# Kernel optimization log

Measured on AMD Instinct MI355X. Metric: run time of the kernel, lower is better.

The kernel has to match this reference:

```python
import jax, jax.numpy as jnp
import numpy as np

K = 5          # kernel_width of the predicted per-pixel kernels
PAD = K // 2   # Unfold padding
CONV_K = 3     # BaseNet: single 3x3 'same' conv, C -> C*K*K


def setup_inputs() -> dict:
    key = jax.random.key(0)
    k1, k2, k3 = jax.random.split(key, 3)
    N, C, H, W = 4, 16, 256, 256
    x = jax.random.normal(k1, (N, C, H, W), dtype=jnp.float32)
    fan_in = C * CONV_K * CONV_K
    conv_w = jax.random.normal(k2, (C * K * K, C, CONV_K, CONV_K), dtype=jnp.float32) / np.sqrt(fan_in).astype(np.float32)
    conv_b = jax.random.normal(k3, (C * K * K,), dtype=jnp.float32) * 0.01
    return {"x": x, "conv_w": conv_w, "conv_b": conv_b}


def _unfold(x):
    # torch.nn.Unfold(K, padding=K//2), reshaped to (N, C, K*K, H, W):
    # patches[n, c, i*K + j, h, w] = x_padded[n, c, h + i, w + j]
    # (channel-major, kernel positions row-major -- matches torch ordering)
    N, C, H, W = x.shape
    xp = jnp.pad(x, ((0, 0), (0, 0), (PAD, PAD), (PAD, PAD)))
    patches = jnp.stack(
        [xp[:, :, i:i + H, j:j + W] for i in range(K) for j in range(K)],
        axis=2,
    )
    return patches  # (N, C, K*K, H, W)


def reference(x, conv_w, conv_b):
    N, C, H, W = x.shape
    # BaseNet: 3x3 'same' conv predicting C*K*K logits per pixel
    out = jax.lax.conv_general_dilated(
        x, conv_w, window_strides=(1, 1), padding='SAME',
        dimension_numbers=('NCHW', 'OIHW', 'NCHW'),
    ) + conv_b[None, :, None, None]
    logits = out.reshape(N, C, K * K, H, W)
    weights = jax.nn.softmax(logits, axis=2)          # softmax over the K*K window
    # einsum('ncuij,ncuij->ncij'): per-pixel weighted sum over the window
    return jnp.einsum('ncuij,ncuij->ncij', _unfold(x), weights)
```

## Files before the change

kernel.cpp:

```cpp
#include <hip/hip_runtime.h>


typedef __bf16 bf16x8 __attribute__((ext_vector_type(8)));
typedef float  f32x16 __attribute__((ext_vector_type(16)));
typedef float  f32x4  __attribute__((ext_vector_type(4)));

#define IMG  256
#define C_IN 16

__device__ __forceinline__ unsigned short f2bf(float f) {
  union { float f; unsigned int u; } v; v.f = f;
  unsigned int u = v.u;
  return (unsigned short)((u + 0x7FFFu + ((u >> 16) & 1u)) >> 16);
}

__global__ __launch_bounds__(256, 2) void kpn_fused(
    const float* __restrict__ x, const float* __restrict__ cw,
    const float* __restrict__ cb, float* __restrict__ out)
{
  __shared__ unsigned short xclf[20 * 20 * 16];
  __shared__ unsigned short xep[20][20][18];
  __shared__ float2 pbl[32][8];

  const int tid  = threadIdx.x;
  const int w0   = blockIdx.x * 16;
  const int h0   = blockIdx.y * 16;
  const int nimg = blockIdx.z;

  {
    int cp = tid & 7, row = tid >> 3;
    float2 v;
    if (row < 25) { v.x = cb[(2 * cp) * 25 + row]; v.y = cb[(2 * cp + 1) * 25 + row]; }
    else          { v.x = -1e30f; v.y = -1e30f; }
    pbl[row][cp] = v;
  }

  char* xclb = (char*)xclf;
  for (int i = tid; i < 3200; i += 256) {
    int ci = i / 200, rem = i % 200, rr = rem / 10, c2 = rem % 10;
    int gh = h0 + rr - 2, gw = w0 + c2 * 2 - 2;
    float vx = 0.f, vy = 0.f;
    if (gh >= 0 && gh < IMG) {
      const float* rowp = x + ((nimg * C_IN + ci) * IMG + gh) * IMG;
      if (gw >= 0 && gw + 1 < IMG) { float2 v = *(const float2*)(rowp + gw); vx = v.x; vy = v.y; }
      else {
        if (gw >= 0 && gw < IMG)         vx = rowp[gw];
        if (gw + 1 >= 0 && gw + 1 < IMG) vy = rowp[gw + 1];
      }
    }
    unsigned short bx = f2bf(vx), by = f2bf(vy);
    int cc = c2 * 2, half = ci >> 3, cil = ci & 7;
    int q0 = rr * 20 + cc, q1 = q0 + 1;
    *(unsigned short*)(xclb + q0 * 32 + ((half ^ (q0 & 1)) << 4) + cil * 2) = bx;
    *(unsigned short*)(xclb + q1 * 32 + ((half ^ (q1 & 1)) << 4) + cil * 2) = by;
    xep[rr][cc][ci] = bx;
    xep[rr][cc + 1][ci] = by;
  }
  __syncthreads();

  const int wave  = tid >> 6;
  const int lane  = tid & 63;
  const int g     = lane >> 5;
  const int n32   = lane & 31;
  const int px    = n32 & 15;
  const int py_in = n32 >> 4;
  const int m     = n32;
  const bool mval = (m < 25);

  int offs[16];
#pragma unroll
  for (int r = 0; r < 16; ++r) {
    int row = 4 * g + (r & 3) + 8 * (r >> 2);
    int du = row / 5, dv = row % 5;
    offs[r] = (row < 25) ? ((du * 20 + dv) * 36) : 0;
  }

  const char* xepb = (const char*)&xep[0][0][0];

  auto epi = [&](const f32x16& A0, const f32x16& A1, int c0, int py) {
    const int cp = c0 >> 1;
    float s0 = 0.f, s1 = 0.f, ws0 = 0.f, ws1 = 0.f;
    const int base = (py * 20 + px) * 36 + c0 * 2;
#pragma unroll
    for (int r = 0; r < 16; ++r) {
      float2 b = pbl[4 * g + (r & 3) + 8 * (r >> 2)][cp];
      float e0 = __expf(A0[r] + b.x);
      float e1 = __expf(A1[r] + b.y);
      s0 += e0; s1 += e1;
      unsigned int u = *(const unsigned int*)(xepb + base + offs[r]);
      union { unsigned int u; float f; } lo, hi;
      lo.u = u << 16; hi.u = u & 0xFFFF0000u;
      ws0 = fmaf(e0, lo.f, ws0);
      ws1 = fmaf(e1, hi.f, ws1);
    }
    s0 += __shfl_xor(s0, 32); s1 += __shfl_xor(s1, 32);
    ws0 += __shfl_xor(ws0, 32); ws1 += __shfl_xor(ws1, 32);
    const int   ch  = c0 + g;
    const float val = (g == 0) ? (ws0 / s0) : (ws1 / s1);
    out[((nimg * C_IN + ch) * IMG + (h0 + py)) * IMG + (w0 + px)] = val;
  };

  for (int pass = 0; pass < 2; ++pass) {
    const int c0 = wave * 4 + pass * 2;

    bf16x8 af[2][9];
#pragma unroll
    for (int cc = 0; cc < 2; ++cc) {
      const float* wp = cw + (((c0 + cc) * 25 + (mval ? m : 0)) * 144 + g * 72);
      float raw[72];
#pragma unroll
      for (int q = 0; q < 18; ++q) {
        f32x4 v = *(const f32x4*)(wp + q * 4);
        raw[q * 4 + 0] = v[0]; raw[q * 4 + 1] = v[1];
        raw[q * 4 + 2] = v[2]; raw[q * 4 + 3] = v[3];
      }
#pragma unroll
      for (int pos = 0; pos < 9; ++pos) {
        bf16x8 f;
#pragma unroll
        for (int j = 0; j < 8; ++j) {
          unsigned short b = mval ? f2bf(raw[j * 9 + pos]) : (unsigned short)0;
          reinterpret_cast<unsigned short*>(&f)[j] = b;
        }
        af[cc][pos] = f;
      }
    }

    for (int ntp = 0; ntp < 4; ++ntp) {
      const int pya = ntp * 4 + py_in;
      const int pyb = pya + 2;
      bf16x8 ba[9], bb[9];
#pragma unroll
      for (int kh = 0; kh < 3; ++kh)
#pragma unroll
        for (int kw = 0; kw < 3; ++kw) {
          int qa = (pya + 1 + kh) * 20 + (px + 1 + kw);
          int qb = (pyb + 1 + kh) * 20 + (px + 1 + kw);
          ba[kh * 3 + kw] = *(const bf16x8*)(xclb + qa * 32 + ((g ^ (qa & 1)) << 4));
          bb[kh * 3 + kw] = *(const bf16x8*)(xclb + qb * 32 + ((g ^ (qb & 1)) << 4));
        }
      f32x16 Aa0{}, Aa1{}, Ab0{}, Ab1{};
#pragma unroll
      for (int pos = 0; pos < 9; ++pos) {
        Aa0 = __builtin_amdgcn_mfma_f32_32x32x16_bf16(af[0][pos], ba[pos], Aa0, 0, 0, 0);
        Aa1 = __builtin_amdgcn_mfma_f32_32x32x16_bf16(af[1][pos], ba[pos], Aa1, 0, 0, 0);
        Ab0 = __builtin_amdgcn_mfma_f32_32x32x16_bf16(af[0][pos], bb[pos], Ab0, 0, 0, 0);
        Ab1 = __builtin_amdgcn_mfma_f32_32x32x16_bf16(af[1][pos], bb[pos], Ab1, 0, 0, 0);
      }
      epi(Aa0, Aa1, c0, pya);
      epi(Ab0, Ab1, c0, pyb);
    }
  }
}

extern "C" void kernel_launch(void* const* d_in, const int* in_sizes, int n_in,
                              void* d_out, int out_size, void* d_ws, size_t ws_size,
                              hipStream_t stream) {
  const float* x  = (const float*)d_in[0];
  const float* cw = (const float*)d_in[1];
  const float* cb = (const float*)d_in[2];
  float* out = (float*)d_out;

  dim3 grid(IMG / 16, IMG / 16, 4);
  kpn_fused<<<grid, 256, 0, stream>>>(x, cw, cb, out);
}
```

Before: 146.7 us.

## Prepack conv weights and bias in a separate kernel, fold bias and log2e into MFMA

Adds a small prepack kernel that converts the conv weights to bf16 MFMA-fragment layout (prescaled by log2e) and lays out the bias per lane in the accumulator format, stored in workspace. The main kernel then loads fragments directly instead of converting per block, seeds the MFMA accumulators with the bias, uses exp2 and a reciprocal, and skips the padded rows in the epilogue. The input tile load is restructured to gather all 16 channels per pixel and pack them with v_cvt_pk_bf16. This removes redundant weight conversion work from every block, at the cost of an extra launch and a different LDS layout without swizzle that may add bank conflicts.

```diff
diff --git a/kernel.cpp b/kernel.cpp
--- a/kernel.cpp
+++ b/kernel.cpp
@@ -3,10 +3,23 @@
 
 typedef __bf16 bf16x8 __attribute__((ext_vector_type(8)));
 typedef float  f32x16 __attribute__((ext_vector_type(16)));
-typedef float  f32x4  __attribute__((ext_vector_type(4)));
-
-#define IMG  256
-#define C_IN 16
+typedef unsigned int uint4v __attribute__((ext_vector_type(4)));
+
+#define IMG   256
+#define C_IN  16
+#define LOG2E 1.4426950408889634f
+
+#if __has_builtin(__builtin_amdgcn_exp2f)
+#define EXP2(x) __builtin_amdgcn_exp2f(x)
+#else
+#define EXP2(x) __expf(0.69314718055994531f * (x))
+#endif
+
+#if __has_builtin(__builtin_amdgcn_rcpf)
+#define RCP(x) __builtin_amdgcn_rcpf(x)
+#else
+#define RCP(x) (1.0f / (x))
+#endif
 
 __device__ __forceinline__ unsigned short f2bf(float f) {
   union { float f; unsigned int u; } v; v.f = f;
@@ -14,47 +27,84 @@
   return (unsigned short)((u + 0x7FFFu + ((u >> 16) & 1u)) >> 16);
 }
 
-__global__ __launch_bounds__(256, 2) void kpn_fused(
-    const float* __restrict__ x, const float* __restrict__ cw,
-    const float* __restrict__ cb, float* __restrict__ out)
+__device__ __forceinline__ unsigned int cvt_pk_bf16(float lo, float hi) {
+  unsigned int r;
+  asm("v_cvt_pk_bf16_f32 %0, %1, %2" : "=v"(r) : "v"(lo), "v"(hi));
+  return r;
+}
+
+__global__ __launch_bounds__(256) void kpn_prepack(
+    const float* __restrict__ cw, const float* __restrict__ cb,
+    unsigned short* __restrict__ apk, float* __restrict__ pb)
 {
-  __shared__ unsigned short xclf[20 * 20 * 16];
-  __shared__ unsigned short xep[20][20][18];
-  __shared__ float2 pbl[32][8];
+  int t = blockIdx.x * 256 + threadIdx.x;
+  if (t < 16 * 9 * 64) {
+    int lane = t & 63, pc = t >> 6;
+    int pos = pc % 9, c = pc / 9;
+    int m = lane & 31, g = lane >> 5;
+    unsigned short v8[8];
+#pragma unroll
+    for (int j = 0; j < 8; ++j) {
+      int ci = 8 * g + j;
+      float v = (m < 25) ? cw[((c * 25 + m) * 16 + ci) * 9 + pos] * LOG2E : 0.f;
+      v8[j] = f2bf(v);
+    }
+    uint4v pk;
+    pk[0] = (unsigned)v8[0] | ((unsigned)v8[1] << 16);
+    pk[1] = (unsigned)v8[2] | ((unsigned)v8[3] << 16);
+    pk[2] = (unsigned)v8[4] | ((unsigned)v8[5] << 16);
+    pk[3] = (unsigned)v8[6] | ((unsigned)v8[7] << 16);
+    *reinterpret_cast<uint4v*>(apk + t * 8) = pk;
+  }
+  int tb = t - 16 * 9 * 64;
+  if (tb >= 0 && tb < 16 * 64) {
+    int lane = tb & 63, c = tb >> 6, g = lane >> 5;
+    f32x16 v;
+#pragma unroll
+    for (int r = 0; r < 16; ++r) {
+      int row = (r & 3) + 8 * (r >> 2) + 4 * g;
+      v[r] = (row < 25) ? cb[c * 25 + row] * LOG2E : -1e30f;
+    }
+    *reinterpret_cast<f32x16*>(pb + tb * 16) = v;
+  }
+}
+
+__global__ __launch_bounds__(256, 2) void kpn_main(
+    const float* __restrict__ x,
+    const unsigned short* __restrict__ apk,
+    const float* __restrict__ pb,
+    float* __restrict__ out)
+{
+  __shared__ unsigned int xcl[400 * 8];
+  __shared__ unsigned int ep[8 * 20 * 24];
 
   const int tid  = threadIdx.x;
   const int w0   = blockIdx.x * 16;
   const int h0   = blockIdx.y * 16;
   const int nimg = blockIdx.z;
 
-  {
-    int cp = tid & 7, row = tid >> 3;
-    float2 v;
-    if (row < 25) { v.x = cb[(2 * cp) * 25 + row]; v.y = cb[(2 * cp + 1) * 25 + row]; }
-    else          { v.x = -1e30f; v.y = -1e30f; }
-    pbl[row][cp] = v;
-  }
-
-  char* xclb = (char*)xclf;
-  for (int i = tid; i < 3200; i += 256) {
-    int ci = i / 200, rem = i % 200, rr = rem / 10, c2 = rem % 10;
-    int gh = h0 + rr - 2, gw = w0 + c2 * 2 - 2;
-    float vx = 0.f, vy = 0.f;
-    if (gh >= 0 && gh < IMG) {
-      const float* rowp = x + ((nimg * C_IN + ci) * IMG + gh) * IMG;
-      if (gw >= 0 && gw + 1 < IMG) { float2 v = *(const float2*)(rowp + gw); vx = v.x; vy = v.y; }
-      else {
-        if (gw >= 0 && gw < IMG)         vx = rowp[gw];
-        if (gw + 1 >= 0 && gw + 1 < IMG) vy = rowp[gw + 1];
-      }
-    }
-    unsigned short bx = f2bf(vx), by = f2bf(vy);
-    int cc = c2 * 2, half = ci >> 3, cil = ci & 7;
-    int q0 = rr * 20 + cc, q1 = q0 + 1;
-    *(unsigned short*)(xclb + q0 * 32 + ((half ^ (q0 & 1)) << 4) + cil * 2) = bx;
-    *(unsigned short*)(xclb + q1 * 32 + ((half ^ (q1 & 1)) << 4) + cil * 2) = by;
-    xep[rr][cc][ci] = bx;
-    xep[rr][cc + 1][ci] = by;
+  for (int p = tid; p < 400; p += 256) {
+    int rr = p / 20, cc = p % 20;
+    int gh = h0 + rr - 2, gw = w0 + cc - 2;
+    float f[16];
+    if (gh >= 0 && gh < IMG && gw >= 0 && gw < IMG) {
+      const float* src = x + (size_t)nimg * C_IN * IMG * IMG + gh * IMG + gw;
+#pragma unroll
+      for (int ci = 0; ci < 16; ++ci) f[ci] = src[ci * IMG * IMG];
+    } else {
+#pragma unroll
+      for (int ci = 0; ci < 16; ++ci) f[ci] = 0.f;
+    }
+    unsigned int u[8];
+#pragma unroll
+    for (int k = 0; k < 8; ++k) u[k] = cvt_pk_bf16(f[2 * k], f[2 * k + 1]);
+    uint4v* dst = reinterpret_cast<uint4v*>(&xcl[p * 8]);
+    uint4v lo, hi;
+    lo[0] = u[0]; lo[1] = u[1]; lo[2] = u[2]; lo[3] = u[3];
+    hi[0] = u[4]; hi[1] = u[5]; hi[2] = u[6]; hi[3] = u[7];
+    dst[0] = lo; dst[1] = hi;
+#pragma unroll
+    for (int k = 0; k < 8; ++k) ep[k * 480 + rr * 24 + cc] = u[k];
   }
   __syncthreads();
 
@@ -64,67 +114,49 @@
   const int n32   = lane & 31;
   const int px    = n32 & 15;
   const int py_in = n32 >> 4;
-  const int m     = n32;
-  const bool mval = (m < 25);
-
-  int offs[16];
-#pragma unroll
-  for (int r = 0; r < 16; ++r) {
+
+  int offs[13];
+#pragma unroll
+  for (int r = 0; r < 13; ++r) {
     int row = 4 * g + (r & 3) + 8 * (r >> 2);
-    int du = row / 5, dv = row % 5;
-    offs[r] = (row < 25) ? ((du * 20 + dv) * 36) : 0;
-  }
-
-  const char* xepb = (const char*)&xep[0][0][0];
+    offs[r] = (row < 25) ? ((row / 5) * 24 + (row % 5)) : 0;
+  }
 
   auto epi = [&](const f32x16& A0, const f32x16& A1, int c0, int py) {
-    const int cp = c0 >> 1;
     float s0 = 0.f, s1 = 0.f, ws0 = 0.f, ws1 = 0.f;
-    const int base = (py * 20 + px) * 36 + c0 * 2;
-#pragma unroll
-    for (int r = 0; r < 16; ++r) {
-      float2 b = pbl[4 * g + (r & 3) + 8 * (r >> 2)][cp];
-      float e0 = __expf(A0[r] + b.x);
-      float e1 = __expf(A1[r] + b.y);
+    const unsigned int* base = &ep[(c0 >> 1) * 480 + py * 24 + px];
+#pragma unroll
+    for (int r = 0; r < 13; ++r) {
+      float e0 = EXP2(A0[r]);
+      float e1 = EXP2(A1[r]);
       s0 += e0; s1 += e1;
-      unsigned int u = *(const unsigned int*)(xepb + base + offs[r]);
+      unsigned int u = base[offs[r]];
       union { unsigned int u; float f; } lo, hi;
       lo.u = u << 16; hi.u = u & 0xFFFF0000u;
       ws0 = fmaf(e0, lo.f, ws0);
       ws1 = fmaf(e1, hi.f, ws1);
     }
-    s0 += __shfl_xor(s0, 32); s1 += __shfl_xor(s1, 32);
+    s0 += __shfl_xor(s0, 32);  s1 += __shfl_xor(s1, 32);
     ws0 += __shfl_xor(ws0, 32); ws1 += __shfl_xor(ws1, 32);
     const int   ch  = c0 + g;
-    const float val = (g == 0) ? (ws0 / s0) : (ws1 / s1);
-    out[((nimg * C_IN + ch) * IMG + (h0 + py)) * IMG + (w0 + px)] = val;
+    const float val = (g == 0) ? (ws0 * RCP(s0)) : (ws1 * RCP(s1));
+    out[(((size_t)nimg * C_IN + ch) * IMG + (h0 + py)) * IMG + (w0 + px)] = val;
   };
+
+  const bf16x8* apv = reinterpret_cast<const bf16x8*>(apk);
+  const f32x16* pbv = reinterpret_cast<const f32x16*>(pb);
 
   for (int pass = 0; pass < 2; ++pass) {
     const int c0 = wave * 4 + pass * 2;
 
-    bf16x8 af[2][9];
-#pragma unroll
-    for (int cc = 0; cc < 2; ++cc) {
-      const float* wp = cw + (((c0 + cc) * 25 + (mval ? m : 0)) * 144 + g * 72);
-      float raw[72];
-#pragma unroll
-      for (int q = 0; q < 18; ++q) {
-        f32x4 v = *(const f32x4*)(wp + q * 4);
-        raw[q * 4 + 0] = v[0]; raw[q * 4 + 1] = v[1];
-        raw[q * 4 + 2] = v[2]; raw[q * 4 + 3] = v[3];
-      }
-#pragma unroll
-      for (int pos = 0; pos < 9; ++pos) {
-        bf16x8 f;
-#pragma unroll
-        for (int j = 0; j < 8; ++j) {
-          unsigned short b = mval ? f2bf(raw[j * 9 + pos]) : (unsigned short)0;
-          reinterpret_cast<unsigned short*>(&f)[j] = b;
-        }
-        af[cc][pos] = f;
-      }
-    }
+    bf16x8 af0[9], af1[9];
+#pragma unroll
+    for (int pos = 0; pos < 9; ++pos) {
+      af0[pos] = apv[(c0 * 9 + pos) * 64 + lane];
+      af1[pos] = apv[((c0 + 1) * 9 + pos) * 64 + lane];
+    }
+    const f32x16 b0 = pbv[c0 * 64 + lane];
+    const f32x16 b1 = pbv[(c0 + 1) * 64 + lane];
 
     for (int ntp = 0; ntp < 4; ++ntp) {
       const int pya = ntp * 4 + py_in;
@@ -136,16 +168,19 @@
         for (int kw = 0; kw < 3; ++kw) {
           int qa = (pya + 1 + kh) * 20 + (px + 1 + kw);
           int qb = (pyb + 1 + kh) * 20 + (px + 1 + kw);
-          ba[kh * 3 + kw] = *(const bf16x8*)(xclb + qa * 32 + ((g ^ (qa & 1)) << 4));
-          bb[kh * 3 + kw] = *(const bf16x8*)(xclb + qb * 32 + ((g ^ (qb & 1)) << 4));
+          ba[kh * 3 + kw] = *reinterpret_cast<const bf16x8*>(&xcl[qa * 8 + g * 4]);
+          bb[kh * 3 + kw] = *reinterpret_cast<const bf16x8*>(&xcl[qb * 8 + g * 4]);
         }
-      f32x16 Aa0{}, Aa1{}, Ab0{}, Ab1{};
-#pragma unroll
-      for (int pos = 0; pos < 9; ++pos) {
-        Aa0 = __builtin_amdgcn_mfma_f32_32x32x16_bf16(af[0][pos], ba[pos], Aa0, 0, 0, 0);
-        Aa1 = __builtin_amdgcn_mfma_f32_32x32x16_bf16(af[1][pos], ba[pos], Aa1, 0, 0, 0);
-        Ab0 = __builtin_amdgcn_mfma_f32_32x32x16_bf16(af[0][pos], bb[pos], Ab0, 0, 0, 0);
-        Ab1 = __builtin_amdgcn_mfma_f32_32x32x16_bf16(af[1][pos], bb[pos], Ab1, 0, 0, 0);
+      f32x16 Aa0 = __builtin_amdgcn_mfma_f32_32x32x16_bf16(af0[0], ba[0], b0, 0, 0, 0);
+      f32x16 Aa1 = __builtin_amdgcn_mfma_f32_32x32x16_bf16(af1[0], ba[0], b1, 0, 0, 0);
+      f32x16 Ab0 = __builtin_amdgcn_mfma_f32_32x32x16_bf16(af0[0], bb[0], b0, 0, 0, 0);
+      f32x16 Ab1 = __builtin_amdgcn_mfma_f32_32x32x16_bf16(af1[0], bb[0], b1, 0, 0, 0);
+#pragma unroll
+      for (int pos = 1; pos < 9; ++pos) {
+        Aa0 = __builtin_amdgcn_mfma_f32_32x32x16_bf16(af0[pos], ba[pos], Aa0, 0, 0, 0);
+        Aa1 = __builtin_amdgcn_mfma_f32_32x32x16_bf16(af1[pos], ba[pos], Aa1, 0, 0, 0);
+        Ab0 = __builtin_amdgcn_mfma_f32_32x32x16_bf16(af0[pos], bb[pos], Ab0, 0, 0, 0);
+        Ab1 = __builtin_amdgcn_mfma_f32_32x32x16_bf16(af1[pos], bb[pos], Ab1, 0, 0, 0);
       }
       epi(Aa0, Aa1, c0, pya);
       epi(Ab0, Ab1, c0, pyb);
@@ -161,6 +196,11 @@
   const float* cb = (const float*)d_in[2];
   float* out = (float*)d_out;
 
+  unsigned short* apk = (unsigned short*)d_ws;
+  float*          pb  = (float*)((char*)d_ws + 16 * 9 * 64 * 8 * 2);
+
+  kpn_prepack<<<40, 256, 0, stream>>>(cw, cb, apk, pb);
+
   dim3 grid(IMG / 16, IMG / 16, 4);
-  kpn_fused<<<grid, 256, 0, stream>>>(x, cw, cb, out);
-}
+  kpn_main<<<grid, 256, 0, stream>>>(x, apk, pb, out);
+}
```

New measurement: 118.0 us. 1.24x faster.
